# Optimization experiments

Hardware: AMD Instinct MI355X
Metric: run time of the kernel (lower is better)

The kernel has to match this reference:

```python
import jax, jax.numpy as jnp
import numpy as np
import math

N_EMB = 768
N_HEAD = 12
N_INNER = 3072
B, T = 2, 2048
EPS = 1e-4


def _gelu_tanh(x):
    return x * 0.5 * (1.0 + jnp.tanh(math.sqrt(2.0 / math.pi) * (x + 0.044715 * x ** 3)))


def _layernorm(x, scale, bias):
    mean = jnp.mean(x, axis=-1, keepdims=True)
    var = jnp.var(x, axis=-1, keepdims=True, ddof=1)  # torch.var default: unbiased
    return scale * ((x - mean) / jnp.sqrt(var + EPS)) + bias


def setup_inputs() -> dict:
    key = jax.random.key(0)
    ks = jax.random.split(key, 16)
    s_attn = 1.0 / math.sqrt(N_EMB)
    s_mlp1 = 1.0 / math.sqrt(N_EMB)
    s_mlp2 = 1.0 / math.sqrt(N_INNER)
    return {
        "x": jax.random.normal(ks[0], (B, T, N_EMB), dtype=jnp.float32),
        "Wq": jax.random.normal(ks[1], (N_EMB, N_EMB), dtype=jnp.float32) * s_attn,
        "bq": jnp.zeros((N_EMB,), jnp.float32),
        "Wk": jax.random.normal(ks[2], (N_EMB, N_EMB), dtype=jnp.float32) * s_attn,
        "bk": jnp.zeros((N_EMB,), jnp.float32),
        "Wv": jax.random.normal(ks[3], (N_EMB, N_EMB), dtype=jnp.float32) * s_attn,
        "bv": jnp.zeros((N_EMB,), jnp.float32),
        "Wo": jax.random.normal(ks[4], (N_EMB, N_EMB), dtype=jnp.float32) * s_attn,
        "bo": jnp.zeros((N_EMB,), jnp.float32),
        "ln1_s": jnp.ones((N_EMB,), jnp.float32),
        "ln1_b": jnp.zeros((N_EMB,), jnp.float32),
        "W1": jax.random.normal(ks[5], (N_EMB, N_INNER), dtype=jnp.float32) * s_mlp1,
        "b1": jnp.zeros((N_INNER,), jnp.float32),
        "W2": jax.random.normal(ks[6], (N_INNER, N_EMB), dtype=jnp.float32) * s_mlp2,
        "b2": jnp.zeros((N_EMB,), jnp.float32),
        "ln2_s": jnp.ones((N_EMB,), jnp.float32),
        "ln2_b": jnp.zeros((N_EMB,), jnp.float32),
    }


def reference(x, Wq, bq, Wk, bk, Wv, bv, Wo, bo, ln1_s, ln1_b, W1, b1, W2, b2, ln2_s, ln2_b):
    Bx, Tx, C = x.shape
    dh = C // N_HEAD
    # QKV projections -> [B, H, T, dh]
    def split_heads(y):
        return y.reshape(Bx, Tx, N_HEAD, dh).transpose(0, 2, 1, 3)
    q = split_heads(x @ Wq + bq)
    k = split_heads(x @ Wk + bk)
    v = split_heads(x @ Wv + bv)
    # naive full-score causal attention (materializes [B,H,T,T])
    scores = jnp.einsum("bhqd,bhkd->bhqk", q, k)
    causal = jnp.tril(jnp.ones((Tx, Tx), dtype=bool))
    scores = jnp.where(causal, scores, -jnp.inf)
    attn = jax.nn.softmax(scores / math.sqrt(dh), axis=-1)
    ctx = jnp.einsum("bhqk,bhkd->bhqd", attn, v)
    ctx = ctx.transpose(0, 2, 1, 3).reshape(Bx, Tx, C)
    attn_out = ctx @ Wo + bo
    # post-norm residual
    h = _layernorm(x + attn_out, ln1_s, ln1_b)
    mlp_out = _gelu_tanh(h @ W1 + b1) @ W2 + b2
    return _layernorm(h + mlp_out, ln2_s, ln2_b)
```

## Files before the change

kernel.cpp:

```cpp
#include <hip/hip_runtime.h>
#include <math.h>

#define TB  2
#define TT  2048
#define TC  768
#define TH  12
#define TDH 64
#define TI  3072
#define TM  (TB*TT)

typedef __attribute__((ext_vector_type(8))) __bf16 bf16x8;
typedef __attribute__((ext_vector_type(4))) __bf16 bf16x4;
typedef __attribute__((ext_vector_type(4))) float  f32x4;

__device__ __forceinline__ float gelu_tanh(float x) {
    float x3 = x * x * x;
    return 0.5f * x * (1.0f + tanhf(0.7978845608028654f * (x + 0.044715f * x3)));
}

__device__ __forceinline__ void gld_lds16(const void* g, void* l) {
    __builtin_amdgcn_global_load_lds(
        (const __attribute__((address_space(1))) unsigned int*)g,
        (__attribute__((address_space(3))) unsigned int*)l,
        16, 0, 0);
}

#define BK 32

template<int BM_, int BN_, int WM_, int WN_>
__global__ __launch_bounds__(256)
void gemm_mfma(const __bf16* __restrict__ A, const __bf16* __restrict__ Bt,
               const float* __restrict__ b0, const float* __restrict__ b1,
               const float* __restrict__ b2, const float* __restrict__ resid,
               float* __restrict__ outf, __bf16* __restrict__ outb,
               int N, int K, size_t wt_stride, size_t out_stride, int ep)
{
    constexpr int WAVES_N = BN_ / WN_;
    constexpr int TMt = WM_ / 16, TNt = WN_ / 16;
    constexpr int AISS = BM_ / 64, BISS = BN_ / 64;
    constexpr int TILE = (BM_ + BN_) * BK;
    __shared__ __align__(16) __bf16 lds[2 * TILE];

    const int tid  = threadIdx.x;
    const int wave = tid >> 6, lane = tid & 63;
    const int wm = wave / WAVES_N, wn = wave % WAVES_N;
    const int m0 = blockIdx.y * BM_, n0 = blockIdx.x * BN_;
    const int z  = blockIdx.z;

    const __bf16* Bz = Bt + (size_t)z * wt_stride;
    const size_t Kb = (size_t)K * 2;
    const char* Ag = (const char*)A + (size_t)m0 * Kb;
    const char* Bg = (const char*)Bz + (size_t)n0 * Kb;
    const int srow = tid >> 2;
    const int scol = ((tid & 3) ^ ((tid >> 4) & 3)) * 16;
    const int wbase = wave * 1024;

    f32x4 acc[TMt][TNt];
    #pragma unroll
    for (int i = 0; i < TMt; ++i)
        #pragma unroll
        for (int j = 0; j < TNt; ++j)
            acc[i][j] = (f32x4){0.f, 0.f, 0.f, 0.f};

    const int arow = wm * WM_ + (lane & 15);
    const int brow = wn * WN_ + (lane & 15);
    const int koff = (((lane >> 4) ^ ((lane >> 2) & 3))) * 8;

    const int nIter = K / BK;

    auto stage = [&](int buf, int k0b) {
        char* base = (char*)lds + (size_t)buf * TILE * 2;
        #pragma unroll
        for (int s = 0; s < AISS; ++s)
            gld_lds16(Ag + (size_t)(srow + 64 * s) * Kb + k0b + scol,
                      base + s * 4096 + wbase);
        char* bbase = base + BM_ * BK * 2;
        #pragma unroll
        for (int s = 0; s < BISS; ++s)
            gld_lds16(Bg + (size_t)(srow + 64 * s) * Kb + k0b + scol,
                      bbase + s * 4096 + wbase);
    };

    stage(0, 0);
    int buf = 0;
    for (int it = 0; it < nIter; ++it) {
        __syncthreads();
        if (it + 1 < nIter) stage(buf ^ 1, (it + 1) * (BK * 2));

        const __bf16* As = lds + (size_t)buf * TILE;
        const __bf16* Bs = As + BM_ * BK;
        bf16x8 af[TMt], bfr[TNt];
        #pragma unroll
        for (int ti = 0; ti < TMt; ++ti)
            af[ti] = *(const bf16x8*)&As[(arow + ti * 16) * BK + koff];
        #pragma unroll
        for (int tj = 0; tj < TNt; ++tj)
            bfr[tj] = *(const bf16x8*)&Bs[(brow + tj * 16) * BK + koff];
        #pragma unroll
        for (int ti = 0; ti < TMt; ++ti)
            #pragma unroll
            for (int tj = 0; tj < TNt; ++tj)
                acc[ti][tj] = __builtin_amdgcn_mfma_f32_16x16x32_bf16(
                    af[ti], bfr[tj], acc[ti][tj], 0, 0, 0);
        buf ^= 1;
    }

    const int lrow = m0 + wm * WM_ + ((lane >> 4) << 2);
    const int lcol = n0 + wn * WN_ + (lane & 15);

    if (ep == 0) {
        const float* bias = (z == 0) ? b0 : (z == 1) ? b1 : b2;
        __bf16* outz = outb + (size_t)z * out_stride;
        if (z < 2) {
            #pragma unroll
            for (int tj = 0; tj < TNt; ++tj) {
                int n = lcol + tj * 16;
                float bj = bias[n];
                int h = n >> 6, d = n & 63;
                #pragma unroll
                for (int ti = 0; ti < TMt; ++ti)
                    #pragma unroll
                    for (int r = 0; r < 4; ++r) {
                        int m = lrow + ti * 16 + r;
                        int b = m >> 11, t = m & (TT - 1);
                        outz[((size_t)(b * TH + h) * TT + t) * TDH + d] =
                            (__bf16)(acc[ti][tj][r] + bj);
                    }
            }
        } else {
            #pragma unroll
            for (int tj = 0; tj < TNt; ++tj) {
                int n = lcol + tj * 16;
                float bj = bias[n];
                int h = n >> 6, d = n & 63;
                #pragma unroll
                for (int ti = 0; ti < TMt; ++ti) {
                    int m = lrow + ti * 16;
                    int b = m >> 11, t0 = m & (TT - 1);
                    bf16x4 pk;
                    #pragma unroll
                    for (int r = 0; r < 4; ++r)
                        pk[r] = (__bf16)(acc[ti][tj][r] + bj);
                    *(bf16x4*)(outz + ((size_t)(b * TH + h) * TDH + d) * TT + t0) = pk;
                }
            }
        }
    } else if (ep == 1) {
        #pragma unroll
        for (int tj = 0; tj < TNt; ++tj) {
            int n = lcol + tj * 16;
            float bj = b0[n];
            #pragma unroll
            for (int ti = 0; ti < TMt; ++ti)
                #pragma unroll
                for (int r = 0; r < 4; ++r) {
                    int m = lrow + ti * 16 + r;
                    outf[(size_t)m * N + n] =
                        acc[ti][tj][r] + bj + resid[(size_t)m * N + n];
                }
        }
    } else {
        #pragma unroll
        for (int tj = 0; tj < TNt; ++tj) {
            int n = lcol + tj * 16;
            float bj = b0[n];
            #pragma unroll
            for (int ti = 0; ti < TMt; ++ti)
                #pragma unroll
                for (int r = 0; r < 4; ++r) {
                    int m = lrow + ti * 16 + r;
                    outb[(size_t)m * N + n] = (__bf16)gelu_tanh(acc[ti][tj][r] + bj);
                }
        }
    }
}

__global__ __launch_bounds__(256)
void prep_kernel(const float* __restrict__ x,
                 const float* __restrict__ Wq, const float* __restrict__ Wk,
                 const float* __restrict__ Wv, const float* __restrict__ Wo,
                 const float* __restrict__ W1, const float* __restrict__ W2,
                 __bf16* __restrict__ x_bf, __bf16* __restrict__ WqkvT,
                 __bf16* __restrict__ WoT, __bf16* __restrict__ W1T,
                 __bf16* __restrict__ W2T)
{
    const size_t WSZ = (size_t)TC * TC;
    int bid = blockIdx.x;
    if (bid < 1536) {
        int i = (bid * 256 + threadIdx.x) * 8;
        float4 a = *(const float4*)(x + i);
        float4 b = *(const float4*)(x + i + 4);
        bf16x8 v;
        v[0] = (__bf16)a.x; v[1] = (__bf16)a.y; v[2] = (__bf16)a.z; v[3] = (__bf16)a.w;
        v[4] = (__bf16)b.x; v[5] = (__bf16)b.y; v[6] = (__bf16)b.z; v[7] = (__bf16)b.w;
        *(bf16x8*)(x_bf + i) = v;
        return;
    }
    bid -= 1536;
    const float* src; __bf16* dst; int K, N, tloc;
    if (bid < 2304) {
        int w = bid / 576; tloc = bid - w * 576;
        K = TC; N = TC;
        src = (w == 0) ? Wq : (w == 1) ? Wk : (w == 2) ? Wv : Wo;
        dst = (w < 3) ? (WqkvT + (size_t)w * WSZ) : WoT;
    } else if (bid < 4608) {
        tloc = bid - 2304; K = TC; N = TI; src = W1; dst = W1T;
    } else {
        tloc = bid - 4608; K = TI; N = TC; src = W2; dst = W2T;
    }
    int tiles_x = N >> 5;
    int n0 = (tloc % tiles_x) * 32, k0 = (tloc / tiles_x) * 32;

    __shared__ float tile[32][33];
    const int tx = threadIdx.x & 31, ty = threadIdx.x >> 5;
    #pragma unroll
    for (int i = 0; i < 32; i += 8)
        tile[ty + i][tx] = src[(size_t)(k0 + ty + i) * N + n0 + tx];
    __syncthreads();
    #pragma unroll
    for (int i = 0; i < 32; i += 8)
        dst[(size_t)(n0 + ty + i) * K + k0 + tx] = (__bf16)tile[tx][ty + i];
}

__global__ __launch_bounds__(256)
void ln_kernel(const float* __restrict__ in, const float* __restrict__ gs,
               const float* __restrict__ gb, float* __restrict__ out,
               __bf16* __restrict__ out_bf)
{
    const int row = blockIdx.x, tid = threadIdx.x;
    const float* r = in + (size_t)row * TC;
    float x0 = r[tid], x1 = r[tid + 256], x2 = r[tid + 512];
    float s = x0 + x1 + x2;
    float q = x0 * x0 + x1 * x1 + x2 * x2;
    #pragma unroll
    for (int off = 32; off > 0; off >>= 1) {
        s += __shfl_down(s, off);
        q += __shfl_down(q, off);
    }
    __shared__ float partial[8];
    __shared__ float stats[2];
    int wid = tid >> 6, lane = tid & 63;
    if (lane == 0) { partial[wid] = s; partial[wid + 4] = q; }
    __syncthreads();
    if (tid == 0) {
        float S = partial[0] + partial[1] + partial[2] + partial[3];
        float Q = partial[4] + partial[5] + partial[6] + partial[7];
        float mean = S * (1.0f / (float)TC);
        float var = (Q - (float)TC * mean * mean) * (1.0f / (float)(TC - 1));
        stats[0] = mean;
        stats[1] = rsqrtf(var + 1e-4f);
    }
    __syncthreads();
    float mean = stats[0], rstd = stats[1];
    float* w = out + (size_t)row * TC;
    float y0 = gs[tid]       * ((x0 - mean) * rstd) + gb[tid];
    float y1 = gs[tid + 256] * ((x1 - mean) * rstd) + gb[tid + 256];
    float y2 = gs[tid + 512] * ((x2 - mean) * rstd) + gb[tid + 512];
    w[tid] = y0; w[tid + 256] = y1; w[tid + 512] = y2;
    if (out_bf) {
        __bf16* wb = out_bf + (size_t)row * TC;
        wb[tid] = (__bf16)y0; wb[tid + 256] = (__bf16)y1; wb[tid + 512] = (__bf16)y2;
    }
}

#define AP 72

__global__ __launch_bounds__(256)
void attn_mfma(const __bf16* __restrict__ Q, const __bf16* __restrict__ K,
               const __bf16* __restrict__ Vt, __bf16* __restrict__ ctx)
{
    __shared__ __align__(16) __bf16 Ks[64 * AP];
    __shared__ __align__(16) __bf16 Vs[64 * AP];
    __shared__ __align__(16) __bf16 Ps[64 * AP];

    const int tid  = threadIdx.x;
    const int wave = tid >> 6, lane = tid & 63;
    const int c = lane & 15, g = lane >> 4;
    const int bh = blockIdx.y;
    const int qi = blockIdx.x;
    const int qt = (qi & 1) ? (31 - (qi >> 1)) : (qi >> 1);
    const int q_glob = qt * 64 + wave * 16 + c;

    const __bf16* Qb = Q  + (size_t)bh * TT * TDH;
    const __bf16* Kb = K  + (size_t)bh * TT * TDH;
    const __bf16* Vb = Vt + (size_t)bh * TDH * TT;

    bf16x8 qf0 = *(const bf16x8*)(Qb + (size_t)q_glob * TDH + g * 8);
    bf16x8 qf1 = *(const bf16x8*)(Qb + (size_t)q_glob * TDH + 32 + g * 8);

    const int srow = tid >> 3;
    const int sc   = (tid & 7) * 8;

    float m_i = -1e30f, l_i = 0.0f;
    f32x4 acc[4];
    #pragma unroll
    for (int m2 = 0; m2 < 4; ++m2) acc[m2] = (f32x4){0.f, 0.f, 0.f, 0.f};

    for (int kt = 0; kt <= qt; ++kt) {
        bf16x8 kv0 = *(const bf16x8*)(Kb + (size_t)(kt * 64 + srow) * TDH + sc);
        bf16x8 kv1 = *(const bf16x8*)(Kb + (size_t)(kt * 64 + srow + 32) * TDH + sc);
        bf16x8 vv0 = *(const bf16x8*)(Vb + (size_t)srow * TT + kt * 64 + sc);
        bf16x8 vv1 = *(const bf16x8*)(Vb + (size_t)(srow + 32) * TT + kt * 64 + sc);
        __syncthreads();
        *(bf16x8*)&Ks[srow * AP + sc]        = kv0;
        *(bf16x8*)&Ks[(srow + 32) * AP + sc] = kv1;
        *(bf16x8*)&Vs[srow * AP + sc]        = vv0;
        *(bf16x8*)&Vs[(srow + 32) * AP + sc] = vv1;
        __syncthreads();

        f32x4 st[4];
        #pragma unroll
        for (int g2 = 0; g2 < 4; ++g2) {
            bf16x8 af0 = *(const bf16x8*)&Ks[(16 * g2 + c) * AP + g * 8];
            bf16x8 af1 = *(const bf16x8*)&Ks[(16 * g2 + c) * AP + 32 + g * 8];
            f32x4 z = (f32x4){0.f, 0.f, 0.f, 0.f};
            z = __builtin_amdgcn_mfma_f32_16x16x32_bf16(af0, qf0, z, 0, 0, 0);
            z = __builtin_amdgcn_mfma_f32_16x16x32_bf16(af1, qf1, z, 0, 0, 0);
            st[g2] = z;
        }

        float sv[4][4];
        float mx = -1e30f;
        if (kt == qt) {
            #pragma unroll
            for (int g2 = 0; g2 < 4; ++g2)
                #pragma unroll
                for (int r = 0; r < 4; ++r) {
                    int kcol = kt * 64 + 16 * g2 + 4 * g + r;
                    float v = (kcol > q_glob) ? -1e30f : st[g2][r] * 0.125f;
                    sv[g2][r] = v;
                    mx = fmaxf(mx, v);
                }
        } else {
            #pragma unroll
            for (int g2 = 0; g2 < 4; ++g2)
                #pragma unroll
                for (int r = 0; r < 4; ++r) {
                    float v = st[g2][r] * 0.125f;
                    sv[g2][r] = v;
                    mx = fmaxf(mx, v);
                }
        }
        mx = fmaxf(mx, __shfl_xor(mx, 16));
        mx = fmaxf(mx, __shfl_xor(mx, 32));
        float nm = fmaxf(m_i, mx);
        float corr = __expf(m_i - nm);
        float ps = 0.f;
        #pragma unroll
        for (int g2 = 0; g2 < 4; ++g2) {
            bf16x4 pk;
            #pragma unroll
            for (int r = 0; r < 4; ++r) {
                float p = __expf(sv[g2][r] - nm);
                ps += p;
                pk[r] = (__bf16)p;
            }
            *(bf16x4*)&Ps[(wave * 16 + c) * AP + 16 * g2 + 4 * g] = pk;
        }
        ps += __shfl_xor(ps, 16);
        ps += __shfl_xor(ps, 32);
        l_i = l_i * corr + ps;
        m_i = nm;
        #pragma unroll
        for (int m2 = 0; m2 < 4; ++m2) {
            acc[m2][0] *= corr; acc[m2][1] *= corr;
            acc[m2][2] *= corr; acc[m2][3] *= corr;
        }

        bf16x8 pf0 = *(const bf16x8*)&Ps[(wave * 16 + c) * AP + g * 8];
        bf16x8 pf1 = *(const bf16x8*)&Ps[(wave * 16 + c) * AP + 32 + g * 8];
        #pragma unroll
        for (int m2 = 0; m2 < 4; ++m2) {
            bf16x8 vf0 = *(const bf16x8*)&Vs[(16 * m2 + c) * AP + g * 8];
            bf16x8 vf1 = *(const bf16x8*)&Vs[(16 * m2 + c) * AP + 32 + g * 8];
            acc[m2] = __builtin_amdgcn_mfma_f32_16x16x32_bf16(vf0, pf0, acc[m2], 0, 0, 0);
            acc[m2] = __builtin_amdgcn_mfma_f32_16x16x32_bf16(vf1, pf1, acc[m2], 0, 0, 0);
        }
    }

    const int b = bh / TH, h = bh - b * TH;
    float inv = 1.0f / l_i;
    #pragma unroll
    for (int m2 = 0; m2 < 4; ++m2) {
        bf16x4 o;
        #pragma unroll
        for (int r = 0; r < 4; ++r)
            o[r] = (__bf16)(acc[m2][r] * inv);
        *(bf16x4*)(ctx + ((size_t)b * TT + q_glob) * TC + h * TDH + 16 * m2 + 4 * g) = o;
    }
}

extern "C" void kernel_launch(void* const* d_in, const int* in_sizes, int n_in,
                              void* d_out, int out_size, void* d_ws, size_t ws_size,
                              hipStream_t stream)
{
    const float* x    = (const float*)d_in[0];
    const float* Wq   = (const float*)d_in[1];
    const float* bq   = (const float*)d_in[2];
    const float* Wk   = (const float*)d_in[3];
    const float* bk   = (const float*)d_in[4];
    const float* Wv   = (const float*)d_in[5];
    const float* bv   = (const float*)d_in[6];
    const float* Wo   = (const float*)d_in[7];
    const float* bo   = (const float*)d_in[8];
    const float* ln1s = (const float*)d_in[9];
    const float* ln1b = (const float*)d_in[10];
    const float* W1   = (const float*)d_in[11];
    const float* b1   = (const float*)d_in[12];
    const float* W2   = (const float*)d_in[13];
    const float* b2   = (const float*)d_in[14];
    const float* ln2s = (const float*)d_in[15];
    const float* ln2b = (const float*)d_in[16];
    float* out = (float*)d_out;

    const size_t MC  = (size_t)TM * TC;
    const size_t MCB = MC * 2;
    const size_t WSZ = (size_t)TC * TC;
    const size_t W12 = (size_t)TC * TI;

    char* W = (char*)d_ws;
    __bf16* qkvb  = (__bf16*)W;
    __bf16* x_bf  = (__bf16*)(W + 3 * MCB);
    float*  tmp1  = (float*)W;
    __bf16* u_bf  = (__bf16*)W;
    float*  h_f32 = (float*)(W + 4 * MCB);
    __bf16* ctxh  = (__bf16*)(W + 6 * MCB);
    __bf16* wts   = (__bf16*)(W + 7 * MCB);
    __bf16* WqkvT = wts;
    __bf16* WoT   = WqkvT + 3 * WSZ;
    __bf16* W1T   = WoT + WSZ;
    __bf16* W2T   = W1T + W12;

    dim3 blk(256);

    prep_kernel<<<dim3(1536 + 6912), blk, 0, stream>>>(
        x, Wq, Wk, Wv, Wo, W1, W2, x_bf, WqkvT, WoT, W1T, W2T);

    gemm_mfma<128, 128, 64, 64><<<dim3(TC / 128, TM / 128, 3), blk, 0, stream>>>(
        x_bf, WqkvT, bq, bk, bv, nullptr, nullptr, qkvb, TC, TC, WSZ, MC, 0);

    attn_mfma<<<dim3(TT / 64, TB * TH), blk, 0, stream>>>(
        qkvb, qkvb + MC, qkvb + 2 * MC, ctxh);

    gemm_mfma<64, 128, 32, 64><<<dim3(TC / 128, TM / 64, 1), blk, 0, stream>>>(
        ctxh, WoT, bo, nullptr, nullptr, x, tmp1, nullptr, TC, TC, 0, 0, 1);

    ln_kernel<<<dim3(TM), blk, 0, stream>>>(tmp1, ln1s, ln1b, h_f32, ctxh);

    gemm_mfma<128, 128, 64, 64><<<dim3(TI / 128, TM / 128, 1), blk, 0, stream>>>(
        ctxh, W1T, b1, nullptr, nullptr, nullptr, nullptr, u_bf, TI, TC, 0, 0, 2);

    gemm_mfma<64, 128, 32, 64><<<dim3(TC / 128, TM / 64, 1), blk, 0, stream>>>(
        u_bf, W2T, b2, nullptr, nullptr, h_f32, out, nullptr, TC, TI, 0, 0, 1);

    ln_kernel<<<dim3(TM), blk, 0, stream>>>(out, ln2s, ln2b, out, nullptr);
}
```

Baseline: 323.5 us.

## Triple-buffer GEMM loads with vmcnt waits, use exp2 softmax, retune GEMM tiles

The GEMM main loop moves from a double-buffered LDS pipeline with a __syncthreads per iteration to a three-stage ring. Two tiles are prefetched ahead, explicit s_waitcnt vmcnt waits cover the outstanding global-to-LDS loads, and raw s_barriers are used, so more memory latency can be hidden. Attention folds log2(e) into the score scale so softmax can use exp2f, and the QKV, Wo and W2 GEMMs get smaller tiles for more blocks. The costs are 1.5x the LDS per block, which may reduce occupancy, and a second barrier per iteration.

```diff
diff --git a/kernel.cpp b/kernel.cpp
--- a/kernel.cpp
+++ b/kernel.cpp
@@ -23,6 +23,17 @@
         (const __attribute__((address_space(1))) unsigned int*)g,
         (__attribute__((address_space(3))) unsigned int*)l,
         16, 0, 0);
+}
+
+template<int N>
+__device__ __forceinline__ void vmcnt_wait() {
+    if constexpr (N == 0)      asm volatile("s_waitcnt vmcnt(0)" ::: "memory");
+    else if constexpr (N == 2) asm volatile("s_waitcnt vmcnt(2)" ::: "memory");
+    else if constexpr (N == 3) asm volatile("s_waitcnt vmcnt(3)" ::: "memory");
+    else if constexpr (N == 4) asm volatile("s_waitcnt vmcnt(4)" ::: "memory");
+    else if constexpr (N == 6) asm volatile("s_waitcnt vmcnt(6)" ::: "memory");
+    else if constexpr (N == 8) asm volatile("s_waitcnt vmcnt(8)" ::: "memory");
+    else static_assert(N == 0, "unsupported vmcnt");
 }
 
 #define BK 32
@@ -38,8 +49,9 @@
     constexpr int WAVES_N = BN_ / WN_;
     constexpr int TMt = WM_ / 16, TNt = WN_ / 16;
     constexpr int AISS = BM_ / 64, BISS = BN_ / 64;
+    constexpr int S    = AISS + BISS;
     constexpr int TILE = (BM_ + BN_) * BK;
-    __shared__ __align__(16) __bf16 lds[2 * TILE];
+    __shared__ __align__(16) __bf16 lds[3 * TILE];
 
     const int tid  = threadIdx.x;
     const int wave = tid >> 6, lane = tid & 63;
@@ -68,8 +80,7 @@
 
     const int nIter = K / BK;
 
-    auto stage = [&](int buf, int k0b) {
-        char* base = (char*)lds + (size_t)buf * TILE * 2;
+    auto stage = [&](char* base, int k0b) {
         #pragma unroll
         for (int s = 0; s < AISS; ++s)
             gld_lds16(Ag + (size_t)(srow + 64 * s) * Kb + k0b + scol,
@@ -81,13 +92,26 @@
                       bbase + s * 4096 + wbase);
     };
 
-    stage(0, 0);
-    int buf = 0;
+    char* P0 = (char*)lds;
+    char* P1 = P0 + (size_t)TILE * 2;
+    char* P2 = P1 + (size_t)TILE * 2;
+
+    stage(P0, 0);
+    if (nIter > 1) stage(P1, BK * 2);
+    __builtin_amdgcn_sched_barrier(0);
+    char* cur = P0; char* n1 = P1; char* n2 = P2;
+
     for (int it = 0; it < nIter; ++it) {
-        __syncthreads();
-        if (it + 1 < nIter) stage(buf ^ 1, (it + 1) * (BK * 2));
-
-        const __bf16* As = lds + (size_t)buf * TILE;
+        if (it + 2 < nIter) stage(n2, (it + 2) * (BK * 2));
+        __builtin_amdgcn_sched_barrier(0);
+        const int rem = nIter - 1 - it;
+        if (rem >= 2)      vmcnt_wait<2 * S>();
+        else if (rem == 1) vmcnt_wait<S>();
+        else               vmcnt_wait<0>();
+        __builtin_amdgcn_s_barrier();
+        __builtin_amdgcn_sched_barrier(0);
+
+        const __bf16* As = (const __bf16*)cur;
         const __bf16* Bs = As + BM_ * BK;
         bf16x8 af[TMt], bfr[TNt];
         #pragma unroll
@@ -102,7 +126,10 @@
             for (int tj = 0; tj < TNt; ++tj)
                 acc[ti][tj] = __builtin_amdgcn_mfma_f32_16x16x32_bf16(
                     af[ti], bfr[tj], acc[ti][tj], 0, 0, 0);
-        buf ^= 1;
+
+        __builtin_amdgcn_sched_barrier(0);
+        __builtin_amdgcn_s_barrier();
+        char* t = cur; cur = n1; n1 = n2; n2 = t;
     }
 
     const int lrow = m0 + wm * WM_ + ((lane >> 4) << 2);
@@ -264,6 +291,7 @@
 }
 
 #define AP 72
+#define ATT_SCALE 0.18033688011112042f
 
 __global__ __launch_bounds__(256)
 void attn_mfma(const __bf16* __restrict__ Q, const __bf16* __restrict__ K,
@@ -327,7 +355,7 @@
                 #pragma unroll
                 for (int r = 0; r < 4; ++r) {
                     int kcol = kt * 64 + 16 * g2 + 4 * g + r;
-                    float v = (kcol > q_glob) ? -1e30f : st[g2][r] * 0.125f;
+                    float v = (kcol > q_glob) ? -1e30f : st[g2][r] * ATT_SCALE;
                     sv[g2][r] = v;
                     mx = fmaxf(mx, v);
                 }
@@ -336,7 +364,7 @@
             for (int g2 = 0; g2 < 4; ++g2)
                 #pragma unroll
                 for (int r = 0; r < 4; ++r) {
-                    float v = st[g2][r] * 0.125f;
+                    float v = st[g2][r] * ATT_SCALE;
                     sv[g2][r] = v;
                     mx = fmaxf(mx, v);
                 }
@@ -344,14 +372,14 @@
         mx = fmaxf(mx, __shfl_xor(mx, 16));
         mx = fmaxf(mx, __shfl_xor(mx, 32));
         float nm = fmaxf(m_i, mx);
-        float corr = __expf(m_i - nm);
+        float corr = exp2f(m_i - nm);
         float ps = 0.f;
         #pragma unroll
         for (int g2 = 0; g2 < 4; ++g2) {
             bf16x4 pk;
             #pragma unroll
             for (int r = 0; r < 4; ++r) {
-                float p = __expf(sv[g2][r] - nm);
+                float p = exp2f(sv[g2][r] - nm);
                 ps += p;
                 pk[r] = (__bf16)p;
             }
@@ -436,13 +464,13 @@
     prep_kernel<<<dim3(1536 + 6912), blk, 0, stream>>>(
         x, Wq, Wk, Wv, Wo, W1, W2, x_bf, WqkvT, WoT, W1T, W2T);
 
-    gemm_mfma<128, 128, 64, 64><<<dim3(TC / 128, TM / 128, 3), blk, 0, stream>>>(
+    gemm_mfma<64, 128, 32, 64><<<dim3(TC / 128, TM / 64, 3), blk, 0, stream>>>(
         x_bf, WqkvT, bq, bk, bv, nullptr, nullptr, qkvb, TC, TC, WSZ, MC, 0);
 
     attn_mfma<<<dim3(TT / 64, TB * TH), blk, 0, stream>>>(
         qkvb, qkvb + MC, qkvb + 2 * MC, ctxh);
 
-    gemm_mfma<64, 128, 32, 64><<<dim3(TC / 128, TM / 64, 1), blk, 0, stream>>>(
+    gemm_mfma<64, 64, 32, 32><<<dim3(TC / 64, TM / 64, 1), blk, 0, stream>>>(
         ctxh, WoT, bo, nullptr, nullptr, x, tmp1, nullptr, TC, TC, 0, 0, 1);
 
     ln_kernel<<<dim3(TM), blk, 0, stream>>>(tmp1, ln1s, ln1b, h_f32, ctxh);
@@ -450,7 +478,7 @@
     gemm_mfma<128, 128, 64, 64><<<dim3(TI / 128, TM / 128, 1), blk, 0, stream>>>(
         ctxh, W1T, b1, nullptr, nullptr, nullptr, nullptr, u_bf, TI, TC, 0, 0, 2);
 
-    gemm_mfma<64, 128, 32, 64><<<dim3(TC / 128, TM / 64, 1), blk, 0, stream>>>(
+    gemm_mfma<64, 64, 32, 32><<<dim3(TC / 64, TM / 64, 1), blk, 0, stream>>>(
         u_bf, W2T, b2, nullptr, nullptr, h_f32, out, nullptr, TC, TI, 0, 0, 1);
 
     ln_kernel<<<dim3(TM), blk, 0, stream>>>(out, ln2s, ln2b, out, nullptr);
```

Result: no change. 326.0 us (+0.8%).
